# Performance work log

Measured on AMD Instinct MI355X. Metric: run time of the kernel, lower is better.

The kernel has to match this reference:

```python
import jax, jax.numpy as jnp
import numpy as np

B, N, DIM = 8, 1024, 768
H, HD = 12, 64
INNER = H * HD
SCALE = HD ** -0.5


def setup_inputs() -> dict:
    key = jax.random.key(0)
    ks = jax.random.split(key, 6)
    return {
        "x": jax.random.normal(ks[0], (B, N, DIM), dtype=jnp.float32),
        "w_qkv": jax.random.normal(ks[1], (DIM, 3 * INNER), dtype=jnp.float32) * 0.02,
        "b_qkv": jax.random.normal(ks[2], (3 * INNER,), dtype=jnp.float32) * 0.02,
        "reattn_weights": jax.random.normal(ks[3], (H, HD, HD), dtype=jnp.float32),
        "w_out": jax.random.normal(ks[4], (INNER, DIM), dtype=jnp.float32) * 0.02,
        "b_out": jax.random.normal(ks[5], (DIM,), dtype=jnp.float32) * 0.02,
    }


def reference(x, w_qkv, b_qkv, reattn_weights, w_out, b_out):
    b, n, _ = x.shape
    qkv = x @ w_qkv + b_qkv  # [b, n, 3*inner]
    q, k, v = jnp.split(qkv, 3, axis=-1)
    # 'b n (h d) -> b h n d'
    def to_heads(t):
        return t.reshape(b, n, H, HD).transpose(0, 2, 1, 3)
    q, k, v = to_heads(q), to_heads(k), to_heads(v)
    dots = jnp.einsum('bhid,bhjd->bhij', q, k) * SCALE
    attn = jax.nn.softmax(dots, axis=-1)
    # einsum 'b h i j, h d e -> b h i j' sums d,e out: per-head scalar scale
    head_scale = reattn_weights.sum(axis=(-1, -2))  # [h]
    attn = attn * head_scale[None, :, None, None]
    out = jnp.einsum('bhij,bhjd->bhid', attn, v)
    out = out.transpose(0, 2, 1, 3).reshape(b, n, INNER)  # 'b h n d -> b n (h d)'
    return out @ w_out + b_out
```

## Files before the change

### kernel.cpp

```cpp
#include <hip/hip_runtime.h>

constexpr int Bn   = 8;
constexpr int Nn   = 1024;
constexpr int DIMn = 768;
constexpr int Hn   = 12;
constexpr int HDn  = 64;
constexpr int INNERn = Hn * HDn;
constexpr int QKVCOLS = 3 * INNERn;
constexpr int Mrows = Bn * Nn;
constexpr float QSCL = 0.18033688011112042f;

typedef float f32x4 __attribute__((ext_vector_type(4)));
typedef __bf16 bf16x8 __attribute__((ext_vector_type(8)));
typedef __bf16 bf16x4 __attribute__((ext_vector_type(4)));

static __device__ __forceinline__ float fexp2(float x) {
#if __has_builtin(__builtin_amdgcn_exp2f)
    return __builtin_amdgcn_exp2f(x);
#else
    return exp2f(x);
#endif
}

static __device__ __forceinline__ void gload16(const void* g, void* l) {
    __builtin_amdgcn_global_load_lds(
        (const __attribute__((address_space(1))) unsigned int*)g,
        (__attribute__((address_space(3))) unsigned int*)l, 16, 0, 0);
}

__global__ __launch_bounds__(256) void head_scale_kernel(
    const float* __restrict__ rw, float* __restrict__ hs)
{
    __shared__ float red[256];
    int h = blockIdx.x;
    const float* p = rw + (size_t)h * (HDn * HDn);
    float s = 0.f;
    for (int i = threadIdx.x; i < HDn * HDn; i += 256) s += p[i];
    red[threadIdx.x] = s;
    __syncthreads();
    #pragma unroll
    for (int off = 128; off > 0; off >>= 1) {
        if ((int)threadIdx.x < off) red[threadIdx.x] += red[threadIdx.x + off];
        __syncthreads();
    }
    if (threadIdx.x == 0) hs[h] = red[0];
}

__global__ __launch_bounds__(256) void convert_x_kernel(
    const float* __restrict__ in, __bf16* __restrict__ outb, int n8)
{
    int i = blockIdx.x * 256 + threadIdx.x;
    if (i >= n8) return;
    const float4* p = (const float4*)(in + (size_t)i * 8);
    float4 a = p[0], b = p[1];
    bf16x8 o = { (__bf16)a.x, (__bf16)a.y, (__bf16)a.z, (__bf16)a.w,
                 (__bf16)b.x, (__bf16)b.y, (__bf16)b.z, (__bf16)b.w };
    *(bf16x8*)(outb + (size_t)i * 8) = o;
}

template<int N>
__global__ __launch_bounds__(256) void transpose_w_kernel(
    const float* __restrict__ w, __bf16* __restrict__ wT)
{
    __shared__ float Ls[64][68];
    int k0 = blockIdx.y * 64, n0 = blockIdx.x * 64;
    int t = threadIdx.x;
    int cc = t & 15, rr = t >> 4;
    #pragma unroll
    for (int it = 0; it < 4; ++it) {
        int row = rr + it * 16;
        float4 v = *(const float4*)(w + (size_t)(k0 + row) * N + n0 + cc * 4);
        *(float4*)(&Ls[row][cc * 4]) = v;
    }
    __syncthreads();
    #pragma unroll
    for (int it = 0; it < 4; ++it) {
        int nr = rr + it * 16;
        bf16x4 o;
        #pragma unroll
        for (int i = 0; i < 4; ++i) o[i] = (__bf16)Ls[cc * 4 + i][nr];
        *(bf16x4*)(wT + (size_t)(n0 + nr) * 768 + k0 + cc * 4) = o;
    }
}

template<int EPI>
__global__ __launch_bounds__(256) void gemm_bf16_kernel(
    const __bf16* __restrict__ A, const __bf16* __restrict__ BT,
    const float* __restrict__ bias,
    __bf16* __restrict__ qb, __bf16* __restrict__ kb, __bf16* __restrict__ vt,
    float* __restrict__ outp)
{
    constexpr int K = 768;
    constexpr int NKT = K / 64;
    __shared__ __attribute__((aligned(16))) __bf16 As[2][128][64];
    __shared__ __attribute__((aligned(16))) __bf16 Bs[2][128][64];

    const int tid = threadIdx.x;
    const int lane = tid & 63, w = tid >> 6;
    const int g = lane >> 4, l16 = lane & 15;
    const int wm = (w >> 1) * 64, wn = (w & 1) * 64;
    const int bid = blockIdx.x;
    const int m0 = (bid & 63) * 128;
    const int n0 = (bid >> 6) * 128;
    const int srl = lane >> 3;
    const int ssl = lane & 7;

    f32x4 acc[4][4] = {};

    auto stage = [&](int kt, int buf) {
        #pragma unroll
        for (int i = 0; i < 4; ++i) {
            int row = w * 32 + i * 8 + srl;
            gload16(A  + (size_t)(m0 + row) * K + kt + ((ssl ^ (row & 7)) << 3),
                    &As[buf][w * 32 + i * 8][0]);
            gload16(BT + (size_t)(n0 + row) * K + kt + ((ssl ^ (row & 7)) << 3),
                    &Bs[buf][w * 32 + i * 8][0]);
        }
    };

    stage(0, 0);
    __syncthreads();

    int cur = 0;
    for (int kti = 0; kti < NKT; ++kti) {
        if (kti < NKT - 1) stage((kti + 1) * 64, cur ^ 1);

        #pragma unroll
        for (int s = 0; s < 2; ++s) {
            bf16x8 af[4], bfr[4];
            #pragma unroll
            for (int f = 0; f < 4; ++f) {
                int ar = wm + f * 16 + l16;
                af[f] = *(const bf16x8*)(&As[cur][ar][((s * 4 + g) ^ (ar & 7)) * 8]);
                int br = wn + f * 16 + l16;
                bfr[f] = *(const bf16x8*)(&Bs[cur][br][((s * 4 + g) ^ (br & 7)) * 8]);
            }
            #pragma unroll
            for (int fa = 0; fa < 4; ++fa)
                #pragma unroll
                for (int fb = 0; fb < 4; ++fb)
                    acc[fa][fb] = __builtin_amdgcn_mfma_f32_16x16x32_bf16(
                        af[fa], bfr[fb], acc[fa][fb], 0, 0, 0);
        }

        __syncthreads();
        cur ^= 1;
    }

    #pragma unroll
    for (int fa = 0; fa < 4; ++fa) {
        #pragma unroll
        for (int fb = 0; fb < 4; ++fb) {
            int n = n0 + wn + fb * 16 + l16;
            float bn = bias[n];
            float v0 = acc[fa][fb][0] + bn;
            float v1 = acc[fa][fb][1] + bn;
            float v2 = acc[fa][fb][2] + bn;
            float v3 = acc[fa][fb][3] + bn;
            int mbase = m0 + wm + fa * 16 + g * 4;
            if (EPI == 0) {
                int which = n / INNERn;
                int rem = n - which * INNERn;
                int hh = rem >> 6, d = rem & 63;
                int bb = mbase >> 10;
                int nn = mbase & 1023;
                size_t bh = (size_t)bb * Hn + hh;
                if (which == 2) {
                    bf16x4 o = { (__bf16)v0, (__bf16)v1, (__bf16)v2, (__bf16)v3 };
                    *(bf16x4*)(vt + (bh * 64 + d) * Nn + nn) = o;
                } else {
                    float sc = (which == 0) ? QSCL : 1.0f;
                    __bf16* dst = (which == 0) ? qb : kb;
                    size_t base = ((bh * Nn + nn) << 6) + d;
                    dst[base]       = (__bf16)(v0 * sc);
                    dst[base + 64]  = (__bf16)(v1 * sc);
                    dst[base + 128] = (__bf16)(v2 * sc);
                    dst[base + 192] = (__bf16)(v3 * sc);
                }
            } else {
                outp[(size_t)(mbase + 0) * INNERn + n] = v0;
                outp[(size_t)(mbase + 1) * INNERn + n] = v1;
                outp[(size_t)(mbase + 2) * INNERn + n] = v2;
                outp[(size_t)(mbase + 3) * INNERn + n] = v3;
            }
        }
    }
}

__global__ __launch_bounds__(256) void attn_mfma_kernel(
    const __bf16* __restrict__ qb, const __bf16* __restrict__ kb,
    const __bf16* __restrict__ vT, const float* __restrict__ hs,
    __bf16* __restrict__ ao)
{
    __shared__ __attribute__((aligned(16))) __bf16 Ks[2][64][64];
    __shared__ __attribute__((aligned(16))) __bf16 Vs[2][64][64];

    const int tid = threadIdx.x;
    const int lane = tid & 63, w = tid >> 6;
    const int g = lane >> 4, l16 = lane & 15;
    const int bid = blockIdx.x;
    const int bh = bid % 96;
    const int qt = bid / 96;
    const int b = bh / Hn, h = bh - b * Hn;

    const __bf16* Qp = qb + ((size_t)bh * Nn + qt * 128 + w * 16) * 64;
    const __bf16* Kp = kb + (size_t)bh * Nn * 64;
    const __bf16* Vp = vT + (size_t)bh * 64 * Nn;

    const int srl = lane >> 3;
    const int ssl = lane & 7;

    bf16x8 qf[2][2];
    #pragma unroll
    for (int t = 0; t < 2; ++t)
        #pragma unroll
        for (int s = 0; s < 2; ++s)
            qf[t][s] = *(const bf16x8*)(Qp + t * 64 * 64 + (size_t)l16 * 64 + s * 32 + g * 8);

    float l0 = 0.f, l1 = 0.f;
    f32x4 oacc0[4] = {}, oacc1[4] = {};

    #pragma unroll
    for (int i = 0; i < 2; ++i) {
        int row = w * 16 + i * 8 + srl;
        gload16(Kp + (size_t)row * 64 + ((ssl ^ (row & 7)) << 3),
                &Ks[0][w * 16 + i * 8][0]);
        gload16(Vp + (size_t)row * Nn + ((ssl ^ (row & 7)) << 3),
                &Vs[0][w * 16 + i * 8][0]);
    }
    __syncthreads();

    int cur = 0;
    for (int jt = 0; jt < Nn / 64; ++jt) {
        if (jt < Nn / 64 - 1) {
            const __bf16* kbase = Kp + (size_t)(jt + 1) * 64 * 64;
            const __bf16* vbase = Vp + (size_t)(jt + 1) * 64;
            #pragma unroll
            for (int i = 0; i < 2; ++i) {
                int row = w * 16 + i * 8 + srl;
                gload16(kbase + (size_t)row * 64 + ((ssl ^ (row & 7)) << 3),
                        &Ks[cur ^ 1][w * 16 + i * 8][0]);
                gload16(vbase + (size_t)row * Nn + ((ssl ^ (row & 7)) << 3),
                        &Vs[cur ^ 1][w * 16 + i * 8][0]);
            }
        }

        f32x4 st0[4] = {}, st1[4] = {};
        #pragma unroll
        for (int s = 0; s < 2; ++s) {
            #pragma unroll
            for (int jf = 0; jf < 4; ++jf) {
                bf16x8 kf = *(const bf16x8*)(
                    &Ks[cur][jf * 16 + l16][((s * 4 + g) ^ (l16 & 7)) * 8]);
                st0[jf] = __builtin_amdgcn_mfma_f32_16x16x32_bf16(kf, qf[0][s], st0[jf], 0, 0, 0);
                st1[jf] = __builtin_amdgcn_mfma_f32_16x16x32_bf16(kf, qf[1][s], st1[jf], 0, 0, 0);
            }
        }

        #pragma unroll
        for (int f = 0; f < 4; ++f)
            #pragma unroll
            for (int r = 0; r < 4; ++r) {
                float p0 = fexp2(st0[f][r]); st0[f][r] = p0; l0 += p0;
                float p1 = fexp2(st1[f][r]); st1[f][r] = p1; l1 += p1;
            }

        bf16x8 pa0[2], pa1[2];
        #pragma unroll
        for (int s = 0; s < 2; ++s) {
            bf16x8 t0 = { (__bf16)st0[2*s][0], (__bf16)st0[2*s][1],
                          (__bf16)st0[2*s][2], (__bf16)st0[2*s][3],
                          (__bf16)st0[2*s+1][0], (__bf16)st0[2*s+1][1],
                          (__bf16)st0[2*s+1][2], (__bf16)st0[2*s+1][3] };
            pa0[s] = t0;
            bf16x8 t1 = { (__bf16)st1[2*s][0], (__bf16)st1[2*s][1],
                          (__bf16)st1[2*s][2], (__bf16)st1[2*s][3],
                          (__bf16)st1[2*s+1][0], (__bf16)st1[2*s+1][1],
                          (__bf16)st1[2*s+1][2], (__bf16)st1[2*s+1][3] };
            pa1[s] = t1;
        }

        #pragma unroll
        for (int s = 0; s < 2; ++s) {
            #pragma unroll
            for (int df = 0; df < 4; ++df) {
                const __bf16* vrow = &Vs[cur][df * 16 + l16][0];
                int c0 = s * 32 + g * 4;
                int i0 = ((c0 >> 3) ^ (l16 & 7)) * 8 + (c0 & 7);
                int c1 = c0 + 16;
                int i1 = ((c1 >> 3) ^ (l16 & 7)) * 8 + (c1 & 7);
                bf16x4 v0 = *(const bf16x4*)(vrow + i0);
                bf16x4 v1 = *(const bf16x4*)(vrow + i1);
                bf16x8 bv = { v0[0], v0[1], v0[2], v0[3], v1[0], v1[1], v1[2], v1[3] };
                oacc0[df] = __builtin_amdgcn_mfma_f32_16x16x32_bf16(pa0[s], bv, oacc0[df], 0, 0, 0);
                oacc1[df] = __builtin_amdgcn_mfma_f32_16x16x32_bf16(pa1[s], bv, oacc1[df], 0, 0, 0);
            }
        }

        __syncthreads();
        cur ^= 1;
    }

    l0 += __shfl_xor(l0, 16);  l0 += __shfl_xor(l0, 32);
    l1 += __shfl_xor(l1, 16);  l1 += __shfl_xor(l1, 32);
    float linv0 = hs[h] / l0;
    float linv1 = hs[h] / l1;

    #pragma unroll
    for (int reg = 0; reg < 4; ++reg) {
        float li0 = __shfl(linv0, 20 * g + reg);
        float li1 = __shfl(linv1, 20 * g + reg);
        int q0 = qt * 128 + w * 16 + g * 4 + reg;
        #pragma unroll
        for (int df = 0; df < 4; ++df) {
            ao[((size_t)b * Nn + q0) * INNERn + h * 64 + df * 16 + l16] =
                (__bf16)(oacc0[df][reg] * li0);
            ao[((size_t)b * Nn + q0 + 64) * INNERn + h * 64 + df * 16 + l16] =
                (__bf16)(oacc1[df][reg] * li1);
        }
    }
}

extern "C" void kernel_launch(void* const* d_in, const int* in_sizes, int n_in,
                              void* d_out, int out_size, void* d_ws, size_t ws_size,
                              hipStream_t stream)
{
    const float* x    = (const float*)d_in[0];
    const float* wqkv = (const float*)d_in[1];
    const float* bqkv = (const float*)d_in[2];
    const float* rw   = (const float*)d_in[3];
    const float* wout = (const float*)d_in[4];
    const float* bout = (const float*)d_in[5];
    float* out = (float*)d_out;
    (void)in_sizes; (void)n_in; (void)out_size; (void)ws_size;

    char* ws = (char*)d_ws;
    size_t off = 0;
    auto alloc = [&](size_t bytes) -> char* {
        char* p = ws + off; off += (bytes + 255) & ~(size_t)255; return p;
    };
    const size_t tsz = (size_t)Mrows * INNERn;
    float*  hsb   = (float*) alloc(Hn * 4);
    __bf16* xb    = (__bf16*)alloc(tsz * 2);
    __bf16* wqkvT = (__bf16*)alloc((size_t)QKVCOLS * DIMn * 2);
    __bf16* woutT = (__bf16*)alloc((size_t)INNERn * DIMn * 2);
    __bf16* qbuf  = (__bf16*)alloc(tsz * 2);
    __bf16* kbuf  = (__bf16*)alloc(tsz * 2);
    __bf16* vTb   = (__bf16*)alloc(tsz * 2);
    __bf16* aob   = (__bf16*)alloc(tsz * 2);

    head_scale_kernel<<<dim3(Hn), dim3(256), 0, stream>>>(rw, hsb);

    convert_x_kernel<<<dim3((int)(tsz / 8 / 256)), dim3(256), 0, stream>>>(x, xb, (int)(tsz / 8));

    transpose_w_kernel<QKVCOLS><<<dim3(QKVCOLS / 64, DIMn / 64), dim3(256), 0, stream>>>(wqkv, wqkvT);
    transpose_w_kernel<INNERn><<<dim3(INNERn / 64, DIMn / 64), dim3(256), 0, stream>>>(wout, woutT);

    gemm_bf16_kernel<0><<<dim3((QKVCOLS / 128) * (Mrows / 128)), dim3(256), 0, stream>>>(
        xb, wqkvT, bqkv, qbuf, kbuf, vTb, nullptr);

    attn_mfma_kernel<<<dim3((Nn / 128) * Bn * Hn), dim3(256), 0, stream>>>(qbuf, kbuf, vTb, hsb, aob);

    gemm_bf16_kernel<1><<<dim3((INNERn / 128) * (Mrows / 128)), dim3(256), 0, stream>>>(
        aob, woutT, bout, nullptr, nullptr, nullptr, out);
}
```

Baseline: 138.3 us.

## Give each attention wave 64 query rows with 128-thread blocks

The attention kernel drops from 4 waves to 2 waves per block. Each wave now processes four 16-row query sub-tiles instead of two, so every K fragment loaded from LDS feeds more MFMAs. K fragments are preloaded per tile, and MFMA sections are wrapped in s_setprio to favour matrix issue. The trade-off is higher register pressure and fewer waves for latency hiding, and each wave issues more of the global loads for the K/V tiles.

```diff
diff --git a/kernel.cpp b/kernel.cpp
--- a/kernel.cpp
+++ b/kernel.cpp
@@ -187,7 +187,7 @@
     }
 }
 
-__global__ __launch_bounds__(256) void attn_mfma_kernel(
+__global__ __launch_bounds__(128) void attn_mfma_kernel(
     const __bf16* __restrict__ qb, const __bf16* __restrict__ kb,
     const __bf16* __restrict__ vT, const float* __restrict__ hs,
     __bf16* __restrict__ ao)
@@ -203,30 +203,30 @@
     const int qt = bid / 96;
     const int b = bh / Hn, h = bh - b * Hn;
 
-    const __bf16* Qp = qb + ((size_t)bh * Nn + qt * 128 + w * 16) * 64;
+    const __bf16* Qp = qb + ((size_t)bh * Nn + qt * 128 + w * 64) * 64;
     const __bf16* Kp = kb + (size_t)bh * Nn * 64;
     const __bf16* Vp = vT + (size_t)bh * 64 * Nn;
 
     const int srl = lane >> 3;
     const int ssl = lane & 7;
 
-    bf16x8 qf[2][2];
-    #pragma unroll
-    for (int t = 0; t < 2; ++t)
+    bf16x8 qf[4][2];
+    #pragma unroll
+    for (int t = 0; t < 4; ++t)
         #pragma unroll
         for (int s = 0; s < 2; ++s)
-            qf[t][s] = *(const bf16x8*)(Qp + t * 64 * 64 + (size_t)l16 * 64 + s * 32 + g * 8);
-
-    float l0 = 0.f, l1 = 0.f;
-    f32x4 oacc0[4] = {}, oacc1[4] = {};
-
-    #pragma unroll
-    for (int i = 0; i < 2; ++i) {
-        int row = w * 16 + i * 8 + srl;
+            qf[t][s] = *(const bf16x8*)(Qp + (size_t)(t * 16 + l16) * 64 + s * 32 + g * 8);
+
+    float l_[4] = {0.f, 0.f, 0.f, 0.f};
+    f32x4 oacc[4][4] = {};
+
+    #pragma unroll
+    for (int i = 0; i < 4; ++i) {
+        int row = w * 32 + i * 8 + srl;
         gload16(Kp + (size_t)row * 64 + ((ssl ^ (row & 7)) << 3),
-                &Ks[0][w * 16 + i * 8][0]);
+                &Ks[0][w * 32 + i * 8][0]);
         gload16(Vp + (size_t)row * Nn + ((ssl ^ (row & 7)) << 3),
-                &Vs[0][w * 16 + i * 8][0]);
+                &Vs[0][w * 32 + i * 8][0]);
     }
     __syncthreads();
 
@@ -236,48 +236,51 @@
             const __bf16* kbase = Kp + (size_t)(jt + 1) * 64 * 64;
             const __bf16* vbase = Vp + (size_t)(jt + 1) * 64;
             #pragma unroll
-            for (int i = 0; i < 2; ++i) {
-                int row = w * 16 + i * 8 + srl;
+            for (int i = 0; i < 4; ++i) {
+                int row = w * 32 + i * 8 + srl;
                 gload16(kbase + (size_t)row * 64 + ((ssl ^ (row & 7)) << 3),
-                        &Ks[cur ^ 1][w * 16 + i * 8][0]);
+                        &Ks[cur ^ 1][w * 32 + i * 8][0]);
                 gload16(vbase + (size_t)row * Nn + ((ssl ^ (row & 7)) << 3),
-                        &Vs[cur ^ 1][w * 16 + i * 8][0]);
-            }
-        }
-
-        f32x4 st0[4] = {}, st1[4] = {};
-        #pragma unroll
-        for (int s = 0; s < 2; ++s) {
-            #pragma unroll
-            for (int jf = 0; jf < 4; ++jf) {
-                bf16x8 kf = *(const bf16x8*)(
+                        &Vs[cur ^ 1][w * 32 + i * 8][0]);
+            }
+        }
+
+        bf16x8 kf[2][4];
+        #pragma unroll
+        for (int s = 0; s < 2; ++s)
+            #pragma unroll
+            for (int jf = 0; jf < 4; ++jf)
+                kf[s][jf] = *(const bf16x8*)(
                     &Ks[cur][jf * 16 + l16][((s * 4 + g) ^ (l16 & 7)) * 8]);
-                st0[jf] = __builtin_amdgcn_mfma_f32_16x16x32_bf16(kf, qf[0][s], st0[jf], 0, 0, 0);
-                st1[jf] = __builtin_amdgcn_mfma_f32_16x16x32_bf16(kf, qf[1][s], st1[jf], 0, 0, 0);
-            }
-        }
-
-        #pragma unroll
-        for (int f = 0; f < 4; ++f)
-            #pragma unroll
-            for (int r = 0; r < 4; ++r) {
-                float p0 = fexp2(st0[f][r]); st0[f][r] = p0; l0 += p0;
-                float p1 = fexp2(st1[f][r]); st1[f][r] = p1; l1 += p1;
-            }
-
-        bf16x8 pa0[2], pa1[2];
-        #pragma unroll
-        for (int s = 0; s < 2; ++s) {
-            bf16x8 t0 = { (__bf16)st0[2*s][0], (__bf16)st0[2*s][1],
-                          (__bf16)st0[2*s][2], (__bf16)st0[2*s][3],
-                          (__bf16)st0[2*s+1][0], (__bf16)st0[2*s+1][1],
-                          (__bf16)st0[2*s+1][2], (__bf16)st0[2*s+1][3] };
-            pa0[s] = t0;
-            bf16x8 t1 = { (__bf16)st1[2*s][0], (__bf16)st1[2*s][1],
-                          (__bf16)st1[2*s][2], (__bf16)st1[2*s][3],
-                          (__bf16)st1[2*s+1][0], (__bf16)st1[2*s+1][1],
-                          (__bf16)st1[2*s+1][2], (__bf16)st1[2*s+1][3] };
-            pa1[s] = t1;
+
+        bf16x8 pa[4][2];
+        #pragma unroll
+        for (int t = 0; t < 4; ++t) {
+            f32x4 st[4] = {};
+            __builtin_amdgcn_s_setprio(1);
+            #pragma unroll
+            for (int s = 0; s < 2; ++s)
+                #pragma unroll
+                for (int jf = 0; jf < 4; ++jf)
+                    st[jf] = __builtin_amdgcn_mfma_f32_16x16x32_bf16(
+                        kf[s][jf], qf[t][s], st[jf], 0, 0, 0);
+            __builtin_amdgcn_s_setprio(0);
+            #pragma unroll
+            for (int f = 0; f < 4; ++f)
+                #pragma unroll
+                for (int r = 0; r < 4; ++r) {
+                    float p = fexp2(st[f][r]);
+                    st[f][r] = p;
+                    l_[t] += p;
+                }
+            pa[t][0] = bf16x8{ (__bf16)st[0][0], (__bf16)st[0][1],
+                               (__bf16)st[0][2], (__bf16)st[0][3],
+                               (__bf16)st[1][0], (__bf16)st[1][1],
+                               (__bf16)st[1][2], (__bf16)st[1][3] };
+            pa[t][1] = bf16x8{ (__bf16)st[2][0], (__bf16)st[2][1],
+                               (__bf16)st[2][2], (__bf16)st[2][3],
+                               (__bf16)st[3][0], (__bf16)st[3][1],
+                               (__bf16)st[3][2], (__bf16)st[3][3] };
         }
 
         #pragma unroll
@@ -292,8 +295,12 @@
                 bf16x4 v0 = *(const bf16x4*)(vrow + i0);
                 bf16x4 v1 = *(const bf16x4*)(vrow + i1);
                 bf16x8 bv = { v0[0], v0[1], v0[2], v0[3], v1[0], v1[1], v1[2], v1[3] };
-                oacc0[df] = __builtin_amdgcn_mfma_f32_16x16x32_bf16(pa0[s], bv, oacc0[df], 0, 0, 0);
-                oacc1[df] = __builtin_amdgcn_mfma_f32_16x16x32_bf16(pa1[s], bv, oacc1[df], 0, 0, 0);
+                __builtin_amdgcn_s_setprio(1);
+                #pragma unroll
+                for (int t = 0; t < 4; ++t)
+                    oacc[t][df] = __builtin_amdgcn_mfma_f32_16x16x32_bf16(
+                        pa[t][s], bv, oacc[t][df], 0, 0, 0);
+                __builtin_amdgcn_s_setprio(0);
             }
         }
 
@@ -301,22 +308,21 @@
         cur ^= 1;
     }
 
-    l0 += __shfl_xor(l0, 16);  l0 += __shfl_xor(l0, 32);
-    l1 += __shfl_xor(l1, 16);  l1 += __shfl_xor(l1, 32);
-    float linv0 = hs[h] / l0;
-    float linv1 = hs[h] / l1;
-
-    #pragma unroll
-    for (int reg = 0; reg < 4; ++reg) {
-        float li0 = __shfl(linv0, 20 * g + reg);
-        float li1 = __shfl(linv1, 20 * g + reg);
-        int q0 = qt * 128 + w * 16 + g * 4 + reg;
-        #pragma unroll
-        for (int df = 0; df < 4; ++df) {
-            ao[((size_t)b * Nn + q0) * INNERn + h * 64 + df * 16 + l16] =
-                (__bf16)(oacc0[df][reg] * li0);
-            ao[((size_t)b * Nn + q0 + 64) * INNERn + h * 64 + df * 16 + l16] =
-                (__bf16)(oacc1[df][reg] * li1);
+    #pragma unroll
+    for (int t = 0; t < 4; ++t) {
+        float lt = l_[t];
+        lt += __shfl_xor(lt, 16);
+        lt += __shfl_xor(lt, 32);
+        float linv = hs[h] / lt;
+        #pragma unroll
+        for (int reg = 0; reg < 4; ++reg) {
+            float li = __shfl(linv, 20 * g + reg);
+            int qrow = qt * 128 + w * 64 + t * 16 + g * 4 + reg;
+            #pragma unroll
+            for (int df = 0; df < 4; ++df) {
+                ao[((size_t)b * Nn + qrow) * INNERn + h * 64 + df * 16 + l16] =
+                    (__bf16)(oacc[t][df][reg] * li);
+            }
         }
     }
 }
@@ -359,7 +365,7 @@
     gemm_bf16_kernel<0><<<dim3((QKVCOLS / 128) * (Mrows / 128)), dim3(256), 0, stream>>>(
         xb, wqkvT, bqkv, qbuf, kbuf, vTb, nullptr);
 
-    attn_mfma_kernel<<<dim3((Nn / 128) * Bn * Hn), dim3(256), 0, stream>>>(qbuf, kbuf, vTb, hsb, aob);
+    attn_mfma_kernel<<<dim3((Nn / 128) * Bn * Hn), dim3(128), 0, stream>>>(qbuf, kbuf, vTb, hsb, aob);
 
     gemm_bf16_kernel<1><<<dim3((INNERn / 128) * (Mrows / 128)), dim3(256), 0, stream>>>(
         aob, woutT, bout, nullptr, nullptr, nullptr, out);
```

After: 159.2 us. +15.1%, slower.

## Use 256x128 GEMM tiles with 8 waves and single-buffered LDS

Applied to the files above, without the earlier changes.

The bf16 GEMM kernels move from 256-thread blocks with 128x128 tiles and a double-buffered LDS pipeline to 512-thread blocks with 256x128 tiles and one LDS buffer. Each block now loads a tile and synchronizes twice per k-step. The larger M tile reuses each B tile across more rows and lowers the block count, and the smaller LDS footprint plus the launch bound of 4 are meant to raise occupancy. In exchange, global-load prefetch no longer overlaps with MFMA work inside a block, so latency hiding depends on other resident blocks.

```diff
diff --git a/kernel.cpp b/kernel.cpp
--- a/kernel.cpp
+++ b/kernel.cpp
@@ -84,7 +84,7 @@
 }
 
 template<int EPI>
-__global__ __launch_bounds__(256) void gemm_bf16_kernel(
+__global__ __launch_bounds__(512, 4) void gemm_bf16_kernel(
     const __bf16* __restrict__ A, const __bf16* __restrict__ BT,
     const float* __restrict__ bias,
     __bf16* __restrict__ qb, __bf16* __restrict__ kb, __bf16* __restrict__ vt,
@@ -92,59 +92,57 @@
 {
     constexpr int K = 768;
     constexpr int NKT = K / 64;
-    __shared__ __attribute__((aligned(16))) __bf16 As[2][128][64];
-    __shared__ __attribute__((aligned(16))) __bf16 Bs[2][128][64];
+    __shared__ __attribute__((aligned(16))) __bf16 As[256][64];
+    __shared__ __attribute__((aligned(16))) __bf16 Bs[128][64];
 
     const int tid = threadIdx.x;
     const int lane = tid & 63, w = tid >> 6;
     const int g = lane >> 4, l16 = lane & 15;
-    const int wm = (w >> 1) * 64, wn = (w & 1) * 64;
+    const int wm = (w >> 1) * 64;
+    const int wn = (w & 1) * 64;
     const int bid = blockIdx.x;
-    const int m0 = (bid & 63) * 128;
-    const int n0 = (bid >> 6) * 128;
+    const int m0 = (bid & 31) * 256;
+    const int n0 = (bid >> 5) * 128;
     const int srl = lane >> 3;
     const int ssl = lane & 7;
 
     f32x4 acc[4][4] = {};
 
-    auto stage = [&](int kt, int buf) {
+    for (int kti = 0; kti < NKT; ++kti) {
+        const int kt = kti * 64;
+        __syncthreads();
         #pragma unroll
         for (int i = 0; i < 4; ++i) {
             int row = w * 32 + i * 8 + srl;
-            gload16(A  + (size_t)(m0 + row) * K + kt + ((ssl ^ (row & 7)) << 3),
-                    &As[buf][w * 32 + i * 8][0]);
+            gload16(A + (size_t)(m0 + row) * K + kt + ((ssl ^ (row & 7)) << 3),
+                    &As[w * 32 + i * 8][0]);
+        }
+        #pragma unroll
+        for (int i = 0; i < 2; ++i) {
+            int row = w * 16 + i * 8 + srl;
             gload16(BT + (size_t)(n0 + row) * K + kt + ((ssl ^ (row & 7)) << 3),
-                    &Bs[buf][w * 32 + i * 8][0]);
-        }
-    };
-
-    stage(0, 0);
-    __syncthreads();
-
-    int cur = 0;
-    for (int kti = 0; kti < NKT; ++kti) {
-        if (kti < NKT - 1) stage((kti + 1) * 64, cur ^ 1);
+                    &Bs[w * 16 + i * 8][0]);
+        }
+        __syncthreads();
 
         #pragma unroll
         for (int s = 0; s < 2; ++s) {
-            bf16x8 af[4], bfr[4];
+            bf16x8 bfr[4];
             #pragma unroll
             for (int f = 0; f < 4; ++f) {
-                int ar = wm + f * 16 + l16;
-                af[f] = *(const bf16x8*)(&As[cur][ar][((s * 4 + g) ^ (ar & 7)) * 8]);
                 int br = wn + f * 16 + l16;
-                bfr[f] = *(const bf16x8*)(&Bs[cur][br][((s * 4 + g) ^ (br & 7)) * 8]);
-            }
-            #pragma unroll
-            for (int fa = 0; fa < 4; ++fa)
+                bfr[f] = *(const bf16x8*)(&Bs[br][((s * 4 + g) ^ (br & 7)) * 8]);
+            }
+            #pragma unroll
+            for (int fa = 0; fa < 4; ++fa) {
+                int ar = wm + fa * 16 + l16;
+                bf16x8 af = *(const bf16x8*)(&As[ar][((s * 4 + g) ^ (ar & 7)) * 8]);
                 #pragma unroll
                 for (int fb = 0; fb < 4; ++fb)
                     acc[fa][fb] = __builtin_amdgcn_mfma_f32_16x16x32_bf16(
-                        af[fa], bfr[fb], acc[fa][fb], 0, 0, 0);
-        }
-
-        __syncthreads();
-        cur ^= 1;
+                        af, bfr[fb], acc[fa][fb], 0, 0, 0);
+            }
+        }
     }
 
     #pragma unroll
@@ -356,11 +354,11 @@
     transpose_w_kernel<QKVCOLS><<<dim3(QKVCOLS / 64, DIMn / 64), dim3(256), 0, stream>>>(wqkv, wqkvT);
     transpose_w_kernel<INNERn><<<dim3(INNERn / 64, DIMn / 64), dim3(256), 0, stream>>>(wout, woutT);
 
-    gemm_bf16_kernel<0><<<dim3((QKVCOLS / 128) * (Mrows / 128)), dim3(256), 0, stream>>>(
+    gemm_bf16_kernel<0><<<dim3((QKVCOLS / 128) * (Mrows / 256)), dim3(512), 0, stream>>>(
         xb, wqkvT, bqkv, qbuf, kbuf, vTb, nullptr);
 
     attn_mfma_kernel<<<dim3((Nn / 128) * Bn * Hn), dim3(256), 0, stream>>>(qbuf, kbuf, vTb, hsb, aob);
 
-    gemm_bf16_kernel<1><<<dim3((INNERn / 128) * (Mrows / 128)), dim3(256), 0, stream>>>(
+    gemm_bf16_kernel<1><<<dim3((INNERn / 128) * (Mrows / 256)), dim3(512), 0, stream>>>(
         aob, woutT, bout, nullptr, nullptr, nullptr, out);
 }
```

New measurement: 149.8 us. 8.3% more time.

## Fuse x conversion into QKV GEMM, merge prep kernels, drop GEMM double buffering

Applied to the files above, without the earlier changes.

Removes the separate fp32-to-bf16 conversion of x. The QKV GEMM now streams fp32 x tiles straight into LDS and converts them to bf16 while building MFMA fragments. The weight transposes and head-scale reduction are merged into one prep launch, cutting launch count. The GEMM drops its LDS double buffer in favour of a single buffer with two barriers per k-tile. This removes load/compute overlap and doubles the bytes of A read from global memory, but frees LDS for occupancy and avoids a full pass over x.

```diff
diff --git a/kernel.cpp b/kernel.cpp
--- a/kernel.cpp
+++ b/kernel.cpp
@@ -28,43 +28,38 @@
         (__attribute__((address_space(3))) unsigned int*)l, 16, 0, 0);
 }
 
-__global__ __launch_bounds__(256) void head_scale_kernel(
-    const float* __restrict__ rw, float* __restrict__ hs)
-{
-    __shared__ float red[256];
-    int h = blockIdx.x;
-    const float* p = rw + (size_t)h * (HDn * HDn);
-    float s = 0.f;
-    for (int i = threadIdx.x; i < HDn * HDn; i += 256) s += p[i];
-    red[threadIdx.x] = s;
-    __syncthreads();
-    #pragma unroll
-    for (int off = 128; off > 0; off >>= 1) {
-        if ((int)threadIdx.x < off) red[threadIdx.x] += red[threadIdx.x + off];
-        __syncthreads();
-    }
-    if (threadIdx.x == 0) hs[h] = red[0];
-}
-
-__global__ __launch_bounds__(256) void convert_x_kernel(
-    const float* __restrict__ in, __bf16* __restrict__ outb, int n8)
-{
-    int i = blockIdx.x * 256 + threadIdx.x;
-    if (i >= n8) return;
-    const float4* p = (const float4*)(in + (size_t)i * 8);
-    float4 a = p[0], b = p[1];
-    bf16x8 o = { (__bf16)a.x, (__bf16)a.y, (__bf16)a.z, (__bf16)a.w,
-                 (__bf16)b.x, (__bf16)b.y, (__bf16)b.z, (__bf16)b.w };
-    *(bf16x8*)(outb + (size_t)i * 8) = o;
-}
-
-template<int N>
-__global__ __launch_bounds__(256) void transpose_w_kernel(
-    const float* __restrict__ w, __bf16* __restrict__ wT)
+__global__ __launch_bounds__(256) void prep_kernel(
+    const float* __restrict__ wqkv, const float* __restrict__ wout,
+    const float* __restrict__ rw,
+    __bf16* __restrict__ wqkvT, __bf16* __restrict__ woutT,
+    float* __restrict__ hs)
 {
     __shared__ float Ls[64][68];
-    int k0 = blockIdx.y * 64, n0 = blockIdx.x * 64;
-    int t = threadIdx.x;
+    __shared__ float red[256];
+    const int bx = blockIdx.x;
+    const int t = threadIdx.x;
+
+    if (bx >= 48) {
+        if (blockIdx.y != 0) return;
+        int h = bx - 48;
+        const float* p = rw + (size_t)h * (HDn * HDn);
+        float s = 0.f;
+        for (int i = t; i < HDn * HDn; i += 256) s += p[i];
+        red[t] = s;
+        __syncthreads();
+        #pragma unroll
+        for (int off = 128; off > 0; off >>= 1) {
+            if (t < off) red[t] += red[t + off];
+            __syncthreads();
+        }
+        if (t == 0) hs[h] = red[0];
+        return;
+    }
+
+    const float* w;  __bf16* wT;  int N, n0;
+    if (bx < 36) { w = wqkv; wT = wqkvT; N = QKVCOLS; n0 = bx * 64; }
+    else         { w = wout; wT = woutT; N = INNERn;  n0 = (bx - 36) * 64; }
+    int k0 = blockIdx.y * 64;
     int cc = t & 15, rr = t >> 4;
     #pragma unroll
     for (int it = 0; it < 4; ++it) {
@@ -83,17 +78,21 @@
     }
 }
 
-template<int EPI>
+template<int EPI, int AF32>
 __global__ __launch_bounds__(256) void gemm_bf16_kernel(
-    const __bf16* __restrict__ A, const __bf16* __restrict__ BT,
+    const void* __restrict__ Ap, const __bf16* __restrict__ BT,
     const float* __restrict__ bias,
     __bf16* __restrict__ qb, __bf16* __restrict__ kb, __bf16* __restrict__ vt,
     float* __restrict__ outp)
 {
     constexpr int K = 768;
-    constexpr int NKT = K / 64;
-    __shared__ __attribute__((aligned(16))) __bf16 As[2][128][64];
-    __shared__ __attribute__((aligned(16))) __bf16 Bs[2][128][64];
+    __shared__ __attribute__((aligned(16))) char AsRaw[AF32 ? 32768 : 16384];
+    __shared__ __attribute__((aligned(16))) __bf16 Bs[128][64];
+
+    const float*  A32 = (const float*)Ap;
+    const __bf16* A16 = (const __bf16*)Ap;
+    float*  As32 = (float*)AsRaw;
+    __bf16* As16 = (__bf16*)AsRaw;
 
     const int tid = threadIdx.x;
     const int lane = tid & 63, w = tid >> 6;
@@ -102,28 +101,41 @@
     const int bid = blockIdx.x;
     const int m0 = (bid & 63) * 128;
     const int n0 = (bid >> 6) * 128;
-    const int srl = lane >> 3;
-    const int ssl = lane & 7;
 
     f32x4 acc[4][4] = {};
 
-    auto stage = [&](int kt, int buf) {
-        #pragma unroll
-        for (int i = 0; i < 4; ++i) {
-            int row = w * 32 + i * 8 + srl;
-            gload16(A  + (size_t)(m0 + row) * K + kt + ((ssl ^ (row & 7)) << 3),
-                    &As[buf][w * 32 + i * 8][0]);
-            gload16(BT + (size_t)(n0 + row) * K + kt + ((ssl ^ (row & 7)) << 3),
-                    &Bs[buf][w * 32 + i * 8][0]);
-        }
-    };
-
-    stage(0, 0);
-    __syncthreads();
-
-    int cur = 0;
-    for (int kti = 0; kti < NKT; ++kti) {
-        if (kti < NKT - 1) stage((kti + 1) * 64, cur ^ 1);
+    for (int kt = 0; kt < K; kt += 64) {
+        __syncthreads();
+        if (AF32) {
+            int lr = lane >> 4, sl = lane & 15;
+            #pragma unroll
+            for (int i = 0; i < 8; ++i) {
+                int rbase = w * 32 + i * 4;
+                int row = rbase + lr;
+                gload16(A32 + (size_t)(m0 + row) * K + kt + ((sl ^ (row & 15)) << 2),
+                        As32 + rbase * 64);
+            }
+        } else {
+            int lr = lane >> 3, sl = lane & 7;
+            #pragma unroll
+            for (int i = 0; i < 4; ++i) {
+                int rbase = w * 32 + i * 8;
+                int row = rbase + lr;
+                gload16(A16 + (size_t)(m0 + row) * K + kt + ((sl ^ (row & 7)) << 3),
+                        As16 + rbase * 64);
+            }
+        }
+        {
+            int lr = lane >> 3, sl = lane & 7;
+            #pragma unroll
+            for (int i = 0; i < 4; ++i) {
+                int rbase = w * 32 + i * 8;
+                int row = rbase + lr;
+                gload16(BT + (size_t)(n0 + row) * K + kt + ((sl ^ (row & 7)) << 3),
+                        &Bs[rbase][0]);
+            }
+        }
+        __syncthreads();
 
         #pragma unroll
         for (int s = 0; s < 2; ++s) {
@@ -131,9 +143,17 @@
             #pragma unroll
             for (int f = 0; f < 4; ++f) {
                 int ar = wm + f * 16 + l16;
-                af[f] = *(const bf16x8*)(&As[cur][ar][((s * 4 + g) ^ (ar & 7)) * 8]);
+                if (AF32) {
+                    const float* base = As32 + ar * 64;
+                    f32x4 va0 = *(const f32x4*)(base + (((s * 8 + g * 2 + 0) ^ l16) << 2));
+                    f32x4 va1 = *(const f32x4*)(base + (((s * 8 + g * 2 + 1) ^ l16) << 2));
+                    af[f] = bf16x8{ (__bf16)va0[0], (__bf16)va0[1], (__bf16)va0[2], (__bf16)va0[3],
+                                    (__bf16)va1[0], (__bf16)va1[1], (__bf16)va1[2], (__bf16)va1[3] };
+                } else {
+                    af[f] = *(const bf16x8*)(As16 + ar * 64 + ((s * 4 + g) ^ (ar & 7)) * 8);
+                }
                 int br = wn + f * 16 + l16;
-                bfr[f] = *(const bf16x8*)(&Bs[cur][br][((s * 4 + g) ^ (br & 7)) * 8]);
+                bfr[f] = *(const bf16x8*)(&Bs[br][((s * 4 + g) ^ (br & 7)) * 8]);
             }
             #pragma unroll
             for (int fa = 0; fa < 4; ++fa)
@@ -142,9 +162,6 @@
                     acc[fa][fb] = __builtin_amdgcn_mfma_f32_16x16x32_bf16(
                         af[fa], bfr[fb], acc[fa][fb], 0, 0, 0);
         }
-
-        __syncthreads();
-        cur ^= 1;
     }
 
     #pragma unroll
@@ -268,16 +285,14 @@
         bf16x8 pa0[2], pa1[2];
         #pragma unroll
         for (int s = 0; s < 2; ++s) {
-            bf16x8 t0 = { (__bf16)st0[2*s][0], (__bf16)st0[2*s][1],
-                          (__bf16)st0[2*s][2], (__bf16)st0[2*s][3],
-                          (__bf16)st0[2*s+1][0], (__bf16)st0[2*s+1][1],
-                          (__bf16)st0[2*s+1][2], (__bf16)st0[2*s+1][3] };
-            pa0[s] = t0;
-            bf16x8 t1 = { (__bf16)st1[2*s][0], (__bf16)st1[2*s][1],
-                          (__bf16)st1[2*s][2], (__bf16)st1[2*s][3],
-                          (__bf16)st1[2*s+1][0], (__bf16)st1[2*s+1][1],
-                          (__bf16)st1[2*s+1][2], (__bf16)st1[2*s+1][3] };
-            pa1[s] = t1;
+            pa0[s] = bf16x8{ (__bf16)st0[2*s][0], (__bf16)st0[2*s][1],
+                             (__bf16)st0[2*s][2], (__bf16)st0[2*s][3],
+                             (__bf16)st0[2*s+1][0], (__bf16)st0[2*s+1][1],
+                             (__bf16)st0[2*s+1][2], (__bf16)st0[2*s+1][3] };
+            pa1[s] = bf16x8{ (__bf16)st1[2*s][0], (__bf16)st1[2*s][1],
+                             (__bf16)st1[2*s][2], (__bf16)st1[2*s][3],
+                             (__bf16)st1[2*s+1][0], (__bf16)st1[2*s+1][1],
+                             (__bf16)st1[2*s+1][2], (__bf16)st1[2*s+1][3] };
         }
 
         #pragma unroll
@@ -341,7 +356,6 @@
     };
     const size_t tsz = (size_t)Mrows * INNERn;
     float*  hsb   = (float*) alloc(Hn * 4);
-    __bf16* xb    = (__bf16*)alloc(tsz * 2);
     __bf16* wqkvT = (__bf16*)alloc((size_t)QKVCOLS * DIMn * 2);
     __bf16* woutT = (__bf16*)alloc((size_t)INNERn * DIMn * 2);
     __bf16* qbuf  = (__bf16*)alloc(tsz * 2);
@@ -349,18 +363,15 @@
     __bf16* vTb   = (__bf16*)alloc(tsz * 2);
     __bf16* aob   = (__bf16*)alloc(tsz * 2);
 
-    head_scale_kernel<<<dim3(Hn), dim3(256), 0, stream>>>(rw, hsb);
-
-    convert_x_kernel<<<dim3((int)(tsz / 8 / 256)), dim3(256), 0, stream>>>(x, xb, (int)(tsz / 8));
-
-    transpose_w_kernel<QKVCOLS><<<dim3(QKVCOLS / 64, DIMn / 64), dim3(256), 0, stream>>>(wqkv, wqkvT);
-    transpose_w_kernel<INNERn><<<dim3(INNERn / 64, DIMn / 64), dim3(256), 0, stream>>>(wout, woutT);
-
-    gemm_bf16_kernel<0><<<dim3((QKVCOLS / 128) * (Mrows / 128)), dim3(256), 0, stream>>>(
-        xb, wqkvT, bqkv, qbuf, kbuf, vTb, nullptr);
-
-    attn_mfma_kernel<<<dim3((Nn / 128) * Bn * Hn), dim3(256), 0, stream>>>(qbuf, kbuf, vTb, hsb, aob);
-
-    gemm_bf16_kernel<1><<<dim3((INNERn / 128) * (Mrows / 128)), dim3(256), 0, stream>>>(
+    prep_kernel<<<dim3(60, 12), dim3(256), 0, stream>>>(
+        wqkv, wout, rw, wqkvT, woutT, hsb);
+
+    gemm_bf16_kernel<0, 1><<<dim3((QKVCOLS / 128) * (Mrows / 128)), dim3(256), 0, stream>>>(
+        x, wqkvT, bqkv, qbuf, kbuf, vTb, nullptr);
+
+    attn_mfma_kernel<<<dim3((Nn / 128) * Bn * Hn), dim3(256), 0, stream>>>(
+        qbuf, kbuf, vTb, hsb, aob);
+
+    gemm_bf16_kernel<1, 0><<<dim3((INNERn / 128) * (Mrows / 128)), dim3(256), 0, stream>>>(
         aob, woutT, bout, nullptr, nullptr, nullptr, out);
 }
```

New measurement: 122.8 us. 1.13x faster.
